# Kernel tuning notes

Measured on AMD Instinct MI355X. Metric: run time of the kernel, lower is better.

## Reference

```python
import jax, jax.numpy as jnp
import numpy as np

B, T, C, H = 2, 2048, 1024, 16
HS = C // H  # 64
EPS = 1e-5


def layer_norm(x, w, b):
    mu = jnp.mean(x, axis=-1, keepdims=True)
    var = jnp.var(x, axis=-1, keepdims=True)
    return (x - mu) * jax.lax.rsqrt(var + EPS) * w + b


def setup_inputs() -> dict:
    key = jax.random.key(0)
    ks = jax.random.split(key, 16)
    s_c = 1.0 / np.sqrt(C)
    s_f = 1.0 / np.sqrt(4 * C)
    u = lambda k, shape, s: jax.random.uniform(k, shape, jnp.float32, -s, s)
    return {
        "x": jax.random.normal(ks[0], (B, T, C), jnp.float32),
        # per-head Q/K/V Linears stacked over heads: [H, C, HS], bias [H, HS]
        "Wq": u(ks[1], (H, C, HS), s_c), "bq": u(ks[2], (H, HS), s_c),
        "Wk": u(ks[3], (H, C, HS), s_c), "bk": u(ks[4], (H, HS), s_c),
        "Wv": u(ks[5], (H, C, HS), s_c), "bv": u(ks[6], (H, HS), s_c),
        "Wp": u(ks[7], (C, C), s_c), "bp": u(ks[8], (C,), s_c),
        "W1": u(ks[9], (C, 4 * C), s_c), "b1": u(ks[10], (4 * C,), s_c),
        "W2": u(ks[11], (4 * C, C), s_f), "b2": u(ks[12], (C,), s_f),
        "ln1_w": jnp.ones((C,), jnp.float32), "ln1_b": jnp.zeros((C,), jnp.float32),
        "ln2_w": jnp.ones((C,), jnp.float32), "ln2_b": jnp.zeros((C,), jnp.float32),
    }


def reference(x, Wq, bq, Wk, bk, Wv, bv, Wp, bp, W1, b1, W2, b2,
              ln1_w, ln1_b, ln2_w, ln2_b):
    # --- pre-norm self-attention ---
    xn = layer_norm(x, ln1_w, ln1_b)
    q = jnp.einsum('btc,hcd->bhtd', xn, Wq) + bq[None, :, None, :]
    k = jnp.einsum('btc,hcd->bhtd', xn, Wk) + bk[None, :, None, :]
    v = jnp.einsum('btc,hcd->bhtd', xn, Wv) + bv[None, :, None, :]
    # NOTE: original scales by C**-0.5 (full embedding dim), not head_size**-0.5
    att = jnp.einsum('bhtd,bhsd->bhts', q, k) * (C ** -0.5)
    att = jax.nn.softmax(att, axis=-1)
    o = jnp.einsum('bhts,bhsd->bhtd', att, v)  # [B,H,T,HS]
    o = jnp.transpose(o, (0, 2, 1, 3)).reshape(B, T, C)  # concat heads
    sa = o @ Wp + bp
    out = x + sa
    # --- pre-norm FFN (exact erf GELU, matching nn.GELU default) ---
    on = layer_norm(out, ln2_w, ln2_b)
    h = jax.nn.gelu(on @ W1 + b1, approximate=False)
    return out + (h @ W2 + b2)
```

## Files before the change

### kernel.cpp

```cpp
#include <hip/hip_runtime.h>
#include <math.h>

#define BB 2
#define TT 2048
#define CC 1024
#define HH 16
#define HS 64
#define MT 4096
#define FF 4096

typedef unsigned short u16;
typedef __bf16 bfrag __attribute__((ext_vector_type(8)));
typedef float f4 __attribute__((ext_vector_type(4)));

#define AS1(p) ((const __attribute__((address_space(1))) void*)(p))
#define AS3(p) ((__attribute__((address_space(3))) void*)(p))

__device__ __forceinline__ u16 f2bf(float f) {
  union { float f; unsigned u; } a; a.f = f;
  return (u16)((a.u + 0x7fffu + ((a.u >> 16) & 1u)) >> 16);
}
__device__ __forceinline__ float bf2f(u16 u) {
  union { unsigned u; float f; } a; a.u = ((unsigned)u) << 16; return a.f;
}

__device__ __forceinline__ int swz128(int byteoff) {
  return byteoff ^ (((byteoff >> 7) & 7) << 4);
}
__device__ __forceinline__ int swzAB(int byteoff) {
  return byteoff ^ (((byteoff >> 7) & 3) << 4);
}

#define XCD_SWZ_2D(BX, BY)                                                     \
  int _fl = (int)blockIdx.y * gridDim.x + blockIdx.x;                          \
  const int _nw = gridDim.x * gridDim.y;                                       \
  _fl = (_fl & 7) * (_nw >> 3) + (_fl >> 3);                                   \
  const int BX = _fl % gridDim.x;                                              \
  const int BY = _fl / gridDim.x;

__global__ void tr_f32_bf16(const float* __restrict__ src, u16* __restrict__ dst,
                            int R, int Cc, long long sb, long long db, int dld) {
  __shared__ float t[32][33];
  const int bz = blockIdx.z;
  const int r0 = blockIdx.y * 32, c0 = blockIdx.x * 32;
  const int tx = threadIdx.x, ty = threadIdx.y;
  const float* s = src + bz * sb;
  u16* d = dst + bz * db;
#pragma unroll
  for (int i = 0; i < 4; i++)
    t[ty + i * 8][tx] = s[(size_t)(r0 + ty + i * 8) * Cc + c0 + tx];
  __syncthreads();
#pragma unroll
  for (int i = 0; i < 4; i++)
    d[(size_t)(c0 + ty + i * 8) * dld + r0 + tx] = f2bf(t[tx][ty + i * 8]);
}

__global__ void tr_bf16(const u16* __restrict__ src, u16* __restrict__ dst,
                        int R, int Cc, long long sb, long long db, int dld) {
  __shared__ u16 t[32][33];
  const int bz = blockIdx.z;
  const int r0 = blockIdx.y * 32, c0 = blockIdx.x * 32;
  const int tx = threadIdx.x, ty = threadIdx.y;
  const u16* s = src + bz * sb;
  u16* d = dst + bz * db;
#pragma unroll
  for (int i = 0; i < 4; i++)
    t[ty + i * 8][tx] = s[(size_t)(r0 + ty + i * 8) * Cc + c0 + tx];
  __syncthreads();
#pragma unroll
  for (int i = 0; i < 4; i++)
    d[(size_t)(c0 + ty + i * 8) * dld + r0 + tx] = t[tx][ty + i * 8];
}

__global__ __launch_bounds__(256) void ln_kernel(
    const float* __restrict__ x, const float* __restrict__ w,
    const float* __restrict__ b, u16* __restrict__ y) {
  const int row = blockIdx.x, tid = threadIdx.x;
  const float4 v = reinterpret_cast<const float4*>(x + (size_t)row * CC)[tid];
  float s = v.x + v.y + v.z + v.w;
  float s2 = v.x * v.x + v.y * v.y + v.z * v.z + v.w * v.w;
#pragma unroll
  for (int off = 32; off >= 1; off >>= 1) {
    s += __shfl_xor(s, off);
    s2 += __shfl_xor(s2, off);
  }
  __shared__ float ps[4], ps2[4];
  const int wave = tid >> 6, lane = tid & 63;
  if (lane == 0) { ps[wave] = s; ps2[wave] = s2; }
  __syncthreads();
  s = ps[0] + ps[1] + ps[2] + ps[3];
  s2 = ps2[0] + ps2[1] + ps2[2] + ps2[3];
  const float mu = s * (1.f / CC);
  const float rstd = rsqrtf(s2 * (1.f / CC) - mu * mu + 1e-5f);
  const float4 wv = reinterpret_cast<const float4*>(w)[tid];
  const float4 bv = reinterpret_cast<const float4*>(b)[tid];
  ushort4 o;
  o.x = f2bf((v.x - mu) * rstd * wv.x + bv.x);
  o.y = f2bf((v.y - mu) * rstd * wv.y + bv.y);
  o.z = f2bf((v.z - mu) * rstd * wv.z + bv.z);
  o.w = f2bf((v.w - mu) * rstd * wv.w + bv.w);
  reinterpret_cast<ushort4*>(y + (size_t)row * CC)[tid] = o;
}

template<int NJ>
__device__ __forceinline__ void gemm_core(
    u16* smem, const u16* __restrict__ A, const u16* __restrict__ Bt,
    int K, int lda, int ldb, int bmi, int bni, f4 (&acc)[4][NJ]) {
  constexpr int BN = NJ * 32;
  constexpr int BBUF = BN * 32;
  u16* As = smem;
  u16* Bs = smem + 3 * 4096;
  const int tid = threadIdx.x;
  const int wave = tid >> 6, lane = tid & 63;
  const int wm = wave >> 1, wn = wave & 1;
  const int lg = lane >> 4, ll = lane & 15;

  const int trow = tid >> 2;
  const int tch  = (tid & 3) ^ ((trow >> 1) & 3);
  const u16* ga = A + (size_t)(bmi * 128 + trow) * lda + tch * 8;
  const u16* gb = Bt + (size_t)(bni * BN + trow) * ldb + tch * 8;
  const size_t g64a = (size_t)64 * lda;
  const size_t g64b = (size_t)64 * ldb;
  const int nt = K >> 5;

  auto GSTAGE = [&](int bi, int kt) {
    u16* la = &As[bi * 4096 + tid * 8];
    u16* lb = &Bs[bi * BBUF + tid * 8];
    const u16* gA = ga + kt * 32;
    const u16* gB = gb + kt * 32;
    __builtin_amdgcn_global_load_lds(AS1(gA), AS3(la), 16, 0, 0);
    __builtin_amdgcn_global_load_lds(AS1(gA + g64a), AS3(la + 2048), 16, 0, 0);
    __builtin_amdgcn_global_load_lds(AS1(gB), AS3(lb), 16, 0, 0);
    if constexpr (NJ == 4)
      __builtin_amdgcn_global_load_lds(AS1(gB + g64b), AS3(lb + 2048), 16, 0, 0);
  };

  GSTAGE(0, 0);
  GSTAGE(1, 1);
  GSTAGE(2, 2);
  int bi = 0;
  for (int t = 0; t < nt; t++) {
    const int ahead = nt - 1 - t;
    if constexpr (NJ == 4) {
      if (ahead >= 2)      asm volatile("s_waitcnt vmcnt(8)" ::: "memory");
      else if (ahead == 1) asm volatile("s_waitcnt vmcnt(4)" ::: "memory");
      else                 asm volatile("s_waitcnt vmcnt(0)" ::: "memory");
    } else {
      if (ahead >= 2)      asm volatile("s_waitcnt vmcnt(6)" ::: "memory");
      else if (ahead == 1) asm volatile("s_waitcnt vmcnt(3)" ::: "memory");
      else                 asm volatile("s_waitcnt vmcnt(0)" ::: "memory");
    }
    __builtin_amdgcn_s_barrier();
    __builtin_amdgcn_sched_barrier(0);

    const char* as_ = (const char*)(As + bi * 4096);
    const char* bs_ = (const char*)(Bs + bi * BBUF);
    bfrag af[4], bf[NJ];
#pragma unroll
    for (int i = 0; i < 4; i++)
      af[i] = *(const bfrag*)(as_ + swzAB((wm * 64 + i * 16 + ll) * 64 + lg * 16));
#pragma unroll
    for (int j = 0; j < NJ; j++)
      bf[j] = *(const bfrag*)(bs_ + swzAB((wn * (BN / 2) + j * 16 + ll) * 64 + lg * 16));

    __builtin_amdgcn_s_setprio(1);
#pragma unroll
    for (int i = 0; i < 4; i++)
#pragma unroll
      for (int j = 0; j < NJ; j++)
        acc[i][j] = __builtin_amdgcn_mfma_f32_16x16x32_bf16(af[i], bf[j], acc[i][j], 0, 0, 0);
    __builtin_amdgcn_s_setprio(0);

    __builtin_amdgcn_sched_barrier(0);
    __builtin_amdgcn_s_barrier();
    if (t + 3 < nt) GSTAGE(bi, t + 3);
    bi = (bi == 2) ? 0 : bi + 1;
  }
}

#define EPI_COORDS                                              \
  const int tid = threadIdx.x;                                  \
  const int wave = tid >> 6, lane = tid & 63;                   \
  const int wm = wave >> 1, wn = wave & 1;                      \
  const int lg = lane >> 4, ll = lane & 15;

__global__ __launch_bounds__(256, 3) void gemm_qkv(
    const u16* __restrict__ A, const u16* __restrict__ Bt,
    const float* __restrict__ bq, const float* __restrict__ bk,
    const float* __restrict__ bv,
    u16* __restrict__ q, u16* __restrict__ k, u16* __restrict__ v) {
  __shared__ u16 smem[24576];
  XCD_SWZ_2D(bx, by)
  f4 acc[4][4] = {};
  gemm_core<4>(smem, A, Bt, CC, CC, CC, by, bx, acc);
  EPI_COORDS
  __syncthreads();
#pragma unroll
  for (int j = 0; j < 4; j++) {
    const int n = bx * 128 + wn * 64 + j * 16 + ll;
    const int sec = n >> 10, nn = n & 1023;
    const float bias = (sec == 0 ? bq : (sec == 1 ? bk : bv))[nn];
    const float scale = (sec == 0) ? 0.045084220027780106f : 1.0f;
#pragma unroll
    for (int i = 0; i < 4; i++)
#pragma unroll
      for (int r = 0; r < 4; r++)
        smem[(wm * 64 + i * 16 + lg * 4 + r) * 136 + wn * 64 + j * 16 + ll] =
            f2bf((acc[i][j][r] + bias) * scale);
  }
  __syncthreads();
  const int rr = tid >> 4, cb = (tid & 15) * 8;
#pragma unroll
  for (int R = 0; R < 8; R++) {
    const int row = R * 16 + rr;
    const int m = by * 128 + row, b = m >> 11, t = m & 2047;
    const int n = bx * 128 + cb;
    const int sec = n >> 10, nn = n & 1023, h = nn >> 6, d = nn & 63;
    u16* dst = sec == 0 ? q : (sec == 1 ? k : v);
    *(uint4*)&dst[(((size_t)b * HH + h) * TT + t) * HS + d] =
        *(const uint4*)&smem[row * 136 + cb];
  }
}

__global__ __launch_bounds__(256, 3) void gemm_ffn1(
    const u16* __restrict__ A, const u16* __restrict__ Bt,
    const float* __restrict__ b1, u16* __restrict__ hb) {
  __shared__ u16 smem[24576];
  XCD_SWZ_2D(bx, by)
  f4 acc[4][4] = {};
  gemm_core<4>(smem, A, Bt, CC, CC, CC, by, bx, acc);
  EPI_COORDS
  __syncthreads();
#pragma unroll
  for (int j = 0; j < 4; j++) {
    const int n = bx * 128 + wn * 64 + j * 16 + ll;
    const float bias = b1[n];
#pragma unroll
    for (int i = 0; i < 4; i++)
#pragma unroll
      for (int r = 0; r < 4; r++) {
        const float t = acc[i][j][r] + bias;
        const float g = 0.5f * t * (1.0f + erff(t * 0.70710678118654752f));
        smem[(wm * 64 + i * 16 + lg * 4 + r) * 136 + wn * 64 + j * 16 + ll] = f2bf(g);
      }
  }
  __syncthreads();
  const int rr = tid >> 4, cb = (tid & 15) * 8;
#pragma unroll
  for (int R = 0; R < 8; R++) {
    const int row = R * 16 + rr;
    *(uint4*)&hb[(size_t)(by * 128 + row) * FF + bx * 128 + cb] =
        *(const uint4*)&smem[row * 136 + cb];
  }
}

__global__ __launch_bounds__(256, 3) void gemm_ffn2sk(
    const u16* __restrict__ A, const u16* __restrict__ Bt,
    u16* __restrict__ p0, u16* __restrict__ p1) {
  __shared__ u16 smem[24576];
  int _fl = ((int)blockIdx.z * gridDim.y + blockIdx.y) * gridDim.x + blockIdx.x;
  const int _nw = gridDim.x * gridDim.y * gridDim.z;
  _fl = (_fl & 7) * (_nw >> 3) + (_fl >> 3);
  const int bx = _fl % gridDim.x;
  const int by = (_fl / gridDim.x) % gridDim.y;
  const int bz = _fl / (gridDim.x * gridDim.y);

  f4 acc[4][4] = {};
  gemm_core<4>(smem, A + bz * 2048, Bt + bz * 2048, 2048, FF, FF, by, bx, acc);
  EPI_COORDS
  __syncthreads();
#pragma unroll
  for (int j = 0; j < 4; j++)
#pragma unroll
    for (int i = 0; i < 4; i++)
#pragma unroll
      for (int r = 0; r < 4; r++)
        smem[(wm * 64 + i * 16 + lg * 4 + r) * 136 + wn * 64 + j * 16 + ll] =
            f2bf(acc[i][j][r]);
  __syncthreads();
  u16* pp = bz ? p1 : p0;
  const int rr = tid >> 4, cb = (tid & 15) * 8;
#pragma unroll
  for (int R = 0; R < 8; R++) {
    const int row = R * 16 + rr;
    *(uint4*)&pp[(size_t)(by * 128 + row) * CC + bx * 128 + cb] =
        *(const uint4*)&smem[row * 136 + cb];
  }
}

__global__ __launch_bounds__(256) void ffn2_reduce(
    const u16* __restrict__ p0, const u16* __restrict__ p1,
    const float* __restrict__ b2, float* __restrict__ dout) {
  const int gid = blockIdx.x * 256 + threadIdx.x;
  const int n0 = (gid * 8) & (CC - 1);
  const uint4 a = ((const uint4*)p0)[gid];
  const uint4 c = ((const uint4*)p1)[gid];
  const u16* au = (const u16*)&a;
  const u16* cu = (const u16*)&c;
  float4 d0 = ((const float4*)dout)[gid * 2];
  float4 d1 = ((const float4*)dout)[gid * 2 + 1];
  const float4 w0 = *(const float4*)&b2[n0];
  const float4 w1 = *(const float4*)&b2[n0 + 4];
  d0.x += w0.x + bf2f(au[0]) + bf2f(cu[0]);
  d0.y += w0.y + bf2f(au[1]) + bf2f(cu[1]);
  d0.z += w0.z + bf2f(au[2]) + bf2f(cu[2]);
  d0.w += w0.w + bf2f(au[3]) + bf2f(cu[3]);
  d1.x += w1.x + bf2f(au[4]) + bf2f(cu[4]);
  d1.y += w1.y + bf2f(au[5]) + bf2f(cu[5]);
  d1.z += w1.z + bf2f(au[6]) + bf2f(cu[6]);
  d1.w += w1.w + bf2f(au[7]) + bf2f(cu[7]);
  ((float4*)dout)[gid * 2] = d0;
  ((float4*)dout)[gid * 2 + 1] = d1;
}

__global__ __launch_bounds__(256, 3) void gemm_proj(
    const u16* __restrict__ A, const u16* __restrict__ Bt,
    const float* __restrict__ bp, const float* __restrict__ x,
    float* __restrict__ outw) {
  __shared__ u16 smem[18432];
  XCD_SWZ_2D(bx, by)
  f4 acc[4][2] = {};
  gemm_core<2>(smem, A, Bt, CC, CC, CC, by, bx, acc);
  EPI_COORDS
#pragma unroll
  for (int i = 0; i < 4; i++)
#pragma unroll
    for (int j = 0; j < 2; j++) {
      const int n = bx * 64 + wn * 32 + j * 16 + ll;
      const float bias = bp[n];
#pragma unroll
      for (int r = 0; r < 4; r++) {
        const int m = by * 128 + wm * 64 + i * 16 + lg * 4 + r;
        const size_t idx = (size_t)m * CC + n;
        outw[idx] = acc[i][j][r] + bias + x[idx];
      }
    }
}

__global__ __launch_bounds__(256, 4) void attn_kernel(
    const u16* __restrict__ Q, const u16* __restrict__ Kb,
    const u16* __restrict__ Vt, u16* __restrict__ Ao) {
  __shared__ __align__(1024) u16 Ks[2][64 * 64];
  __shared__ __align__(1024) u16 Vs[2][64 * 64];
  __shared__ __align__(1024) u16 Ps[4][16 * 64];
  const int bh = blockIdx.y, qt = blockIdx.x;
  const int tid = threadIdx.x, wave = tid >> 6, lane = tid & 63;
  const int lg = lane >> 4, ll = lane & 15;

  bfrag qf[2];
  const u16* Qb = Q + ((size_t)bh * TT + qt * 64 + wave * 16) * HS;
#pragma unroll
  for (int dc = 0; dc < 2; dc++)
    qf[dc] = *(const bfrag*)&Qb[ll * HS + dc * 32 + lg * 8];

  f4 o[4] = {};
  float mrun = -INFINITY, lrun = 0.f;

  const int trow = tid >> 3;
  const int tch  = (tid & 7) ^ (trow & 7);
  const u16* gk = Kb + ((size_t)bh * TT + trow) * HS + tch * 8;
  const u16* gv = Vt + ((size_t)bh * HS + trow) * TT + tch * 8;

  char* const pw = (char*)Ps[wave];

#define STAGE(bufi, stt)                                                          \
  do {                                                                            \
    u16* lk = &Ks[bufi][tid * 8];                                                 \
    u16* lv = &Vs[bufi][tid * 8];                                                 \
    __builtin_amdgcn_global_load_lds(AS1(gk + (size_t)(stt) * HS), AS3(lk), 16, 0, 0); \
    __builtin_amdgcn_global_load_lds(AS1(gk + (size_t)(stt) * HS + 32 * HS), AS3(lk + 2048), 16, 0, 0); \
    __builtin_amdgcn_global_load_lds(AS1(gv + (stt)), AS3(lv), 16, 0, 0);         \
    __builtin_amdgcn_global_load_lds(AS1(gv + (stt) + (size_t)32 * TT), AS3(lv + 2048), 16, 0, 0); \
  } while (0)

  STAGE(0, 0);
  int cur = 0;

  for (int st = 0; st < TT; st += 64) {
    if (st + 64 < TT) {
      STAGE(cur ^ 1, st + 64);
      asm volatile("s_waitcnt vmcnt(4)" ::: "memory");
    } else {
      asm volatile("s_waitcnt vmcnt(0)" ::: "memory");
    }
    __builtin_amdgcn_s_barrier();
    __builtin_amdgcn_sched_barrier(0);

    const char* kbuf = (const char*)Ks[cur];
    const char* vbuf = (const char*)Vs[cur];

    f4 p[4];
#pragma unroll
    for (int kb = 0; kb < 4; kb++) {
      const int row = kb * 16 + ll;
      const bfrag k0 = *(const bfrag*)(kbuf + swz128(row * 128 + lg * 16));
      const bfrag k1 = *(const bfrag*)(kbuf + swz128(row * 128 + 64 + lg * 16));
      f4 z = {0.f, 0.f, 0.f, 0.f};
      z = __builtin_amdgcn_mfma_f32_16x16x32_bf16(k0, qf[0], z, 0, 0, 0);
      p[kb] = __builtin_amdgcn_mfma_f32_16x16x32_bf16(k1, qf[1], z, 0, 0, 0);
    }

    {
      float pm = p[0][0];
#pragma unroll
      for (int kb = 0; kb < 4; kb++)
#pragma unroll
        for (int r = 0; r < 4; r++)
          if (kb | r) pm = fmaxf(pm, p[kb][r]);
      pm = fmaxf(pm, __shfl_xor(pm, 16));
      pm = fmaxf(pm, __shfl_xor(pm, 32));
      const float mn = fmaxf(mrun, pm);
      const float al = exp2f(mrun - mn);
      mrun = mn;
      float rs = 0.f;
#pragma unroll
      for (int kb = 0; kb < 4; kb++)
#pragma unroll
        for (int r = 0; r < 4; r++) {
          const float e = exp2f(p[kb][r] - mn);
          p[kb][r] = e;
          rs += e;
        }
      rs += __shfl_xor(rs, 16);
      rs += __shfl_xor(rs, 32);
      lrun = lrun * al + rs;
#pragma unroll
      for (int fo = 0; fo < 4; fo++) o[fo] *= al;
#pragma unroll
      for (int kb = 0; kb < 4; kb++) {
        union { uint2 v; __bf16 h[4]; } w;
        w.h[0] = (__bf16)p[kb][0];
        w.h[1] = (__bf16)p[kb][1];
        w.h[2] = (__bf16)p[kb][2];
        w.h[3] = (__bf16)p[kb][3];
        *(uint2*)(pw + swz128(ll * 128 + kb * 32 + lg * 8)) = w.v;
      }
    }

#pragma unroll
    for (int ks = 0; ks < 2; ks++) {
      const bfrag pb = *(const bfrag*)(pw + swz128(ll * 128 + ks * 64 + lg * 16));
#pragma unroll
      for (int fo = 0; fo < 4; fo++) {
        const bfrag vf = *(const bfrag*)(vbuf + swz128((fo * 16 + ll) * 128 + ks * 64 + lg * 16));
        o[fo] = __builtin_amdgcn_mfma_f32_16x16x32_bf16(vf, pb, o[fo], 0, 0, 0);
      }
    }

    __builtin_amdgcn_sched_barrier(0);
    __builtin_amdgcn_s_barrier();
    cur ^= 1;
  }
#undef STAGE

  const int b = bh >> 4, h = bh & 15;
  const float inv = 1.0f / lrun;
  const int t = qt * 64 + wave * 16 + ll;
#pragma unroll
  for (int fo = 0; fo < 4; fo++) {
    union { uint2 v; __bf16 hh[4]; } w;
    w.hh[0] = (__bf16)(o[fo][0] * inv);
    w.hh[1] = (__bf16)(o[fo][1] * inv);
    w.hh[2] = (__bf16)(o[fo][2] * inv);
    w.hh[3] = (__bf16)(o[fo][3] * inv);
    *(uint2*)&Ao[((size_t)b * TT + t) * CC + h * HS + fo * 16 + lg * 4] = w.v;
  }
}

extern "C" void kernel_launch(void* const* d_in, const int* in_sizes, int n_in,
                              void* d_out, int out_size, void* d_ws, size_t ws_size,
                              hipStream_t stream) {
  const float* x    = (const float*)d_in[0];
  const float* Wq   = (const float*)d_in[1];
  const float* bq   = (const float*)d_in[2];
  const float* Wk   = (const float*)d_in[3];
  const float* bk   = (const float*)d_in[4];
  const float* Wv   = (const float*)d_in[5];
  const float* bv   = (const float*)d_in[6];
  const float* Wp   = (const float*)d_in[7];
  const float* bp   = (const float*)d_in[8];
  const float* W1   = (const float*)d_in[9];
  const float* b1   = (const float*)d_in[10];
  const float* W2   = (const float*)d_in[11];
  const float* b2   = (const float*)d_in[12];
  const float* ln1w = (const float*)d_in[13];
  const float* ln1b = (const float*)d_in[14];
  const float* ln2w = (const float*)d_in[15];
  const float* ln2b = (const float*)d_in[16];
  float* dout = (float*)d_out;

  char* ws = (char*)d_ws;
  u16* wqkv = (u16*)(ws + 0);
  u16* wpt  = (u16*)(ws + 6291456);
  u16* w1t  = (u16*)(ws + 8388608);
  u16* w2t  = (u16*)(ws + 16777216);
  u16* xn   = (u16*)(ws + 25165824);
  u16* qb   = (u16*)(ws + 33554432);
  u16* kb   = (u16*)(ws + 41943040);
  u16* vb   = (u16*)(ws + 50331648);
  u16* vt   = (u16*)(ws + 58720256);
  u16* ao   = (u16*)(ws + 67108864);
  u16* hb   = qb;
  u16* pk0  = (u16*)(ws + 0);
  u16* pk1  = (u16*)(ws + 8388608);

  dim3 blk256(256);
  dim3 blkT(32, 8);

  tr_f32_bf16<<<dim3(2, 32, 16), blkT, 0, stream>>>(Wq, wqkv,               1024,   64, 65536LL, 65536LL, 1024);
  tr_f32_bf16<<<dim3(2, 32, 16), blkT, 0, stream>>>(Wk, wqkv + 1024 * 1024, 1024,   64, 65536LL, 65536LL, 1024);
  tr_f32_bf16<<<dim3(2, 32, 16), blkT, 0, stream>>>(Wv, wqkv + 2048 * 1024, 1024,   64, 65536LL, 65536LL, 1024);
  tr_f32_bf16<<<dim3(32, 32, 1),  blkT, 0, stream>>>(Wp, wpt, 1024, 1024, 0LL, 0LL, 1024);
  tr_f32_bf16<<<dim3(128, 32, 1), blkT, 0, stream>>>(W1, w1t, 1024, 4096, 0LL, 0LL, 1024);
  tr_f32_bf16<<<dim3(32, 128, 1), blkT, 0, stream>>>(W2, w2t, 4096, 1024, 0LL, 0LL, 4096);

  ln_kernel<<<dim3(MT), blk256, 0, stream>>>(x, ln1w, ln1b, xn);

  gemm_qkv<<<dim3(24, 32), blk256, 0, stream>>>(xn, wqkv, bq, bk, bv, qb, kb, vb);

  tr_bf16<<<dim3(2, 64, 32), blkT, 0, stream>>>(vb, vt, 2048, 64, 131072LL, 131072LL, 2048);

  attn_kernel<<<dim3(32, 32), blk256, 0, stream>>>(qb, kb, vt, ao);

  gemm_proj<<<dim3(16, 32), blk256, 0, stream>>>(ao, wpt, bp, x, dout);

  ln_kernel<<<dim3(MT), blk256, 0, stream>>>(dout, ln2w, ln2b, xn);

  gemm_ffn1<<<dim3(32, 32), blk256, 0, stream>>>(xn, w1t, b1, hb);
  gemm_ffn2sk<<<dim3(8, 32, 2), blk256, 0, stream>>>(hb, w2t, pk0, pk1);
  ffn2_reduce<<<dim3(MT * CC / 8 / 256), blk256, 0, stream>>>(pk0, pk1, b2, dout);
}
```

Before: 277.5 us.

## Rewrite attention with 32x32 MFMA tiles, register-resident P, and lazy rescale

The attention kernel now uses 32x32x16 bf16 MFMAs, with each wave covering 32 query rows, so a block handles 128 queries and the grid is halved. The softmax probabilities are packed to bf16 with v_cvt_pk_bf16_f32 and rearranged with v_permlane32_swap instead of a round trip through LDS. The running-max rescale of the output and denominator is skipped when no lane's max increased, and the block index is remapped to group heads for K/V cache reuse. This raises per-thread register use and lowers the occupancy bound from 4 to 2 blocks, with fewer blocks in flight.

```diff
diff --git a/kernel.cpp b/kernel.cpp
--- a/kernel.cpp
+++ b/kernel.cpp
@@ -12,6 +12,7 @@
 typedef unsigned short u16;
 typedef __bf16 bfrag __attribute__((ext_vector_type(8)));
 typedef float f4 __attribute__((ext_vector_type(4)));
+typedef float f16v __attribute__((ext_vector_type(16)));
 
 #define AS1(p) ((const __attribute__((address_space(1))) void*)(p))
 #define AS3(p) ((__attribute__((address_space(3))) void*)(p))
@@ -337,23 +338,27 @@
     }
 }
 
-__global__ __launch_bounds__(256, 4) void attn_kernel(
+__global__ __launch_bounds__(256, 2) void attn_kernel(
     const u16* __restrict__ Q, const u16* __restrict__ Kb,
     const u16* __restrict__ Vt, u16* __restrict__ Ao) {
   __shared__ __align__(1024) u16 Ks[2][64 * 64];
   __shared__ __align__(1024) u16 Vs[2][64 * 64];
-  __shared__ __align__(1024) u16 Ps[4][16 * 64];
-  const int bh = blockIdx.y, qt = blockIdx.x;
+
+  const int fl = (int)blockIdx.y * gridDim.x + blockIdx.x;
+  const int idx = fl >> 3;
+  const int bh = (idx >> 4) * 8 + (fl & 7);
+  const int qt = idx & 15;
+
   const int tid = threadIdx.x, wave = tid >> 6, lane = tid & 63;
-  const int lg = lane >> 4, ll = lane & 15;
-
-  bfrag qf[2];
-  const u16* Qb = Q + ((size_t)bh * TT + qt * 64 + wave * 16) * HS;
-#pragma unroll
-  for (int dc = 0; dc < 2; dc++)
-    qf[dc] = *(const bfrag*)&Qb[ll * HS + dc * 32 + lg * 8];
-
-  f4 o[4] = {};
+  const int l31 = lane & 31, hi = lane >> 5;
+
+  bfrag qf[4];
+  const u16* Qb = Q + ((size_t)bh * TT + qt * 128 + wave * 32) * HS;
+#pragma unroll
+  for (int t = 0; t < 4; t++)
+    qf[t] = *(const bfrag*)&Qb[l31 * HS + t * 16 + hi * 8];
+
+  f16v o0 = {}, o1 = {};
   float mrun = -INFINITY, lrun = 0.f;
 
   const int trow = tid >> 3;
@@ -361,7 +366,18 @@
   const u16* gk = Kb + ((size_t)bh * TT + trow) * HS + tch * 8;
   const u16* gv = Vt + ((size_t)bh * HS + trow) * TT + tch * 8;
 
-  char* const pw = (char*)Ps[wave];
+  int koff[2][4], voff[2][2][2];
+#pragma unroll
+  for (int sub = 0; sub < 2; sub++) {
+#pragma unroll
+    for (int t = 0; t < 4; t++)
+      koff[sub][t] = swz128((sub * 32 + l31) * 128 + t * 32 + hi * 16);
+#pragma unroll
+    for (int dh = 0; dh < 2; dh++)
+#pragma unroll
+      for (int ks = 0; ks < 2; ks++)
+        voff[dh][sub][ks] = swz128((dh * 32 + l31) * 128 + sub * 64 + ks * 32 + hi * 16);
+  }
 
 #define STAGE(bufi, stt)                                                          \
   do {                                                                            \
@@ -389,63 +405,78 @@
     const char* kbuf = (const char*)Ks[cur];
     const char* vbuf = (const char*)Vs[cur];
 
-    f4 p[4];
-#pragma unroll
-    for (int kb = 0; kb < 4; kb++) {
-      const int row = kb * 16 + ll;
-      const bfrag k0 = *(const bfrag*)(kbuf + swz128(row * 128 + lg * 16));
-      const bfrag k1 = *(const bfrag*)(kbuf + swz128(row * 128 + 64 + lg * 16));
-      f4 z = {0.f, 0.f, 0.f, 0.f};
-      z = __builtin_amdgcn_mfma_f32_16x16x32_bf16(k0, qf[0], z, 0, 0, 0);
-      p[kb] = __builtin_amdgcn_mfma_f32_16x16x32_bf16(k1, qf[1], z, 0, 0, 0);
-    }
-
-    {
-      float pm = p[0][0];
-#pragma unroll
-      for (int kb = 0; kb < 4; kb++)
-#pragma unroll
-        for (int r = 0; r < 4; r++)
-          if (kb | r) pm = fmaxf(pm, p[kb][r]);
-      pm = fmaxf(pm, __shfl_xor(pm, 16));
-      pm = fmaxf(pm, __shfl_xor(pm, 32));
+    f16v s0 = {}, s1 = {};
+#pragma unroll
+    for (int t = 0; t < 4; t++) {
+      const bfrag kf0 = *(const bfrag*)(kbuf + koff[0][t]);
+      s0 = __builtin_amdgcn_mfma_f32_32x32x16_bf16(kf0, qf[t], s0, 0, 0, 0);
+    }
+#pragma unroll
+    for (int t = 0; t < 4; t++) {
+      const bfrag kf1 = *(const bfrag*)(kbuf + koff[1][t]);
+      s1 = __builtin_amdgcn_mfma_f32_32x32x16_bf16(kf1, qf[t], s1, 0, 0, 0);
+    }
+
+    float t8[8];
+#pragma unroll
+    for (int j = 0; j < 8; j++) t8[j] = fmaxf(s0[j], s0[j + 8]);
+#pragma unroll
+    for (int j = 0; j < 8; j++) t8[j] = fmaxf(t8[j], fmaxf(s1[j], s1[j + 8]));
+#pragma unroll
+    for (int j = 0; j < 4; j++) t8[j] = fmaxf(t8[j], t8[j + 4]);
+    float pm = fmaxf(fmaxf(t8[0], t8[1]), fmaxf(t8[2], t8[3]));
+    pm = fmaxf(pm, __shfl_xor(pm, 32));
+
+    if (!__all((int)(pm <= mrun))) {
       const float mn = fmaxf(mrun, pm);
       const float al = exp2f(mrun - mn);
       mrun = mn;
-      float rs = 0.f;
-#pragma unroll
-      for (int kb = 0; kb < 4; kb++)
-#pragma unroll
-        for (int r = 0; r < 4; r++) {
-          const float e = exp2f(p[kb][r] - mn);
-          p[kb][r] = e;
-          rs += e;
-        }
-      rs += __shfl_xor(rs, 16);
-      rs += __shfl_xor(rs, 32);
-      lrun = lrun * al + rs;
-#pragma unroll
-      for (int fo = 0; fo < 4; fo++) o[fo] *= al;
-#pragma unroll
-      for (int kb = 0; kb < 4; kb++) {
-        union { uint2 v; __bf16 h[4]; } w;
-        w.h[0] = (__bf16)p[kb][0];
-        w.h[1] = (__bf16)p[kb][1];
-        w.h[2] = (__bf16)p[kb][2];
-        w.h[3] = (__bf16)p[kb][3];
-        *(uint2*)(pw + swz128(ll * 128 + kb * 32 + lg * 8)) = w.v;
+      lrun *= al;
+#pragma unroll
+      for (int j = 0; j < 16; j++) { o0[j] *= al; o1[j] *= al; }
+    }
+
+    unsigned pf[2][2][4];
+    float rs = 0.f;
+#pragma unroll
+    for (int j = 0; j < 16; j++) { s0[j] = exp2f(s0[j] - mrun); rs += s0[j]; }
+#pragma unroll
+    for (int j = 0; j < 16; j++) { s1[j] = exp2f(s1[j] - mrun); rs += s1[j]; }
+    rs += __shfl_xor(rs, 32);
+    lrun += rs;
+
+#pragma unroll
+    for (int sub = 0; sub < 2; sub++) {
+      const f16v& sv = sub ? s1 : s0;
+      unsigned a0, a1, a2, a3, a4, a5, a6, a7;
+      asm("v_cvt_pk_bf16_f32 %0, %1, %2" : "=v"(a0) : "v"(sv[0]),  "v"(sv[1]));
+      asm("v_cvt_pk_bf16_f32 %0, %1, %2" : "=v"(a1) : "v"(sv[2]),  "v"(sv[3]));
+      asm("v_cvt_pk_bf16_f32 %0, %1, %2" : "=v"(a2) : "v"(sv[4]),  "v"(sv[5]));
+      asm("v_cvt_pk_bf16_f32 %0, %1, %2" : "=v"(a3) : "v"(sv[6]),  "v"(sv[7]));
+      asm("v_cvt_pk_bf16_f32 %0, %1, %2" : "=v"(a4) : "v"(sv[8]),  "v"(sv[9]));
+      asm("v_cvt_pk_bf16_f32 %0, %1, %2" : "=v"(a5) : "v"(sv[10]), "v"(sv[11]));
+      asm("v_cvt_pk_bf16_f32 %0, %1, %2" : "=v"(a6) : "v"(sv[12]), "v"(sv[13]));
+      asm("v_cvt_pk_bf16_f32 %0, %1, %2" : "=v"(a7) : "v"(sv[14]), "v"(sv[15]));
+      asm("v_permlane32_swap_b32 %0, %1" : "+v"(a2), "+v"(a0));
+      asm("v_permlane32_swap_b32 %0, %1" : "+v"(a3), "+v"(a1));
+      asm("v_permlane32_swap_b32 %0, %1" : "+v"(a6), "+v"(a4));
+      asm("v_permlane32_swap_b32 %0, %1" : "+v"(a7), "+v"(a5));
+      pf[sub][0][0] = a0; pf[sub][0][1] = a1; pf[sub][0][2] = a2; pf[sub][0][3] = a3;
+      pf[sub][1][0] = a4; pf[sub][1][1] = a5; pf[sub][1][2] = a6; pf[sub][1][3] = a7;
+    }
+
+#pragma unroll
+    for (int sub = 0; sub < 2; sub++)
+#pragma unroll
+      for (int ks = 0; ks < 2; ks++) {
+        union { unsigned u[4]; bfrag b; } pb;
+        pb.u[0] = pf[sub][ks][0]; pb.u[1] = pf[sub][ks][1];
+        pb.u[2] = pf[sub][ks][2]; pb.u[3] = pf[sub][ks][3];
+        const bfrag vf0 = *(const bfrag*)(vbuf + voff[0][sub][ks]);
+        o0 = __builtin_amdgcn_mfma_f32_32x32x16_bf16(vf0, pb.b, o0, 0, 0, 0);
+        const bfrag vf1 = *(const bfrag*)(vbuf + voff[1][sub][ks]);
+        o1 = __builtin_amdgcn_mfma_f32_32x32x16_bf16(vf1, pb.b, o1, 0, 0, 0);
       }
-    }
-
-#pragma unroll
-    for (int ks = 0; ks < 2; ks++) {
-      const bfrag pb = *(const bfrag*)(pw + swz128(ll * 128 + ks * 64 + lg * 16));
-#pragma unroll
-      for (int fo = 0; fo < 4; fo++) {
-        const bfrag vf = *(const bfrag*)(vbuf + swz128((fo * 16 + ll) * 128 + ks * 64 + lg * 16));
-        o[fo] = __builtin_amdgcn_mfma_f32_16x16x32_bf16(vf, pb, o[fo], 0, 0, 0);
-      }
-    }
 
     __builtin_amdgcn_sched_barrier(0);
     __builtin_amdgcn_s_barrier();
@@ -455,15 +486,20 @@
 
   const int b = bh >> 4, h = bh & 15;
   const float inv = 1.0f / lrun;
-  const int t = qt * 64 + wave * 16 + ll;
-#pragma unroll
-  for (int fo = 0; fo < 4; fo++) {
-    union { uint2 v; __bf16 hh[4]; } w;
-    w.hh[0] = (__bf16)(o[fo][0] * inv);
-    w.hh[1] = (__bf16)(o[fo][1] * inv);
-    w.hh[2] = (__bf16)(o[fo][2] * inv);
-    w.hh[3] = (__bf16)(o[fo][3] * inv);
-    *(uint2*)&Ao[((size_t)b * TT + t) * CC + h * HS + fo * 16 + lg * 4] = w.v;
+  const int t = qt * 128 + wave * 32 + l31;
+  u16* aorow = Ao + ((size_t)b * TT + t) * CC + h * HS;
+#pragma unroll
+  for (int dh = 0; dh < 2; dh++) {
+    const f16v& ov = dh ? o1 : o0;
+#pragma unroll
+    for (int rq = 0; rq < 4; rq++) {
+      union { uint2 v; __bf16 hh[4]; } w;
+      w.hh[0] = (__bf16)(ov[rq * 4 + 0] * inv);
+      w.hh[1] = (__bf16)(ov[rq * 4 + 1] * inv);
+      w.hh[2] = (__bf16)(ov[rq * 4 + 2] * inv);
+      w.hh[3] = (__bf16)(ov[rq * 4 + 3] * inv);
+      *(uint2*)&aorow[dh * 32 + rq * 8 + hi * 4] = w.v;
+    }
   }
 }
 
@@ -520,7 +556,7 @@
 
   tr_bf16<<<dim3(2, 64, 32), blkT, 0, stream>>>(vb, vt, 2048, 64, 131072LL, 131072LL, 2048);
 
-  attn_kernel<<<dim3(32, 32), blk256, 0, stream>>>(qb, kb, vt, ao);
+  attn_kernel<<<dim3(16, 32), blk256, 0, stream>>>(qb, kb, vt, ao);
 
   gemm_proj<<<dim3(16, 32), blk256, 0, stream>>>(ao, wpt, bp, x, dout);
 
```

Result: no change. 272.1 us (median of 2 runs) (-2.0%).
